# Kernel optimization log

Measured on AMD Instinct MI355X. Metric: run time of the kernel, lower is better.

The kernel has to match this reference:

```python
import jax, jax.numpy as jnp
import numpy as np

DEPTH = 12
N_FEATURES = 512
BATCH = 16384
N_NODES = 2 ** DEPTH - 1   # 4095 internal nodes, concatenated level-by-level
N_LEAVES = 2 ** DEPTH      # 4096


def setup_inputs() -> dict:
    key = jax.random.key(0)
    k_x, k_w, k_b, k_s, k_l = jax.random.split(key, 5)
    x_input = jax.random.normal(k_x, (BATCH, N_FEATURES), dtype=jnp.float32)
    # Per-level Linear(n_features, 2**d) weights concatenated on the output dim:
    # level d occupies rows [2**d - 1, 2**(d+1) - 1).
    bound = 1.0 / np.sqrt(N_FEATURES)  # torch Linear default init scale
    W_all = jax.random.uniform(k_w, (N_NODES, N_FEATURES), dtype=jnp.float32,
                               minval=-bound, maxval=bound)
    b_all = jax.random.uniform(k_b, (N_NODES,), dtype=jnp.float32,
                               minval=-bound, maxval=bound)
    # original uses max(randn, 1) -> positive steepness >= 1
    s_all = jax.random.uniform(k_s, (N_NODES,), dtype=jnp.float32,
                               minval=1.0, maxval=2.0)
    leaves = jax.random.normal(k_l, (N_LEAVES,), dtype=jnp.float32)
    return {"x_input": x_input, "W_all": W_all, "b_all": b_all,
            "s_all": s_all, "leaves": leaves}


def reference(x_input, W_all, b_all, s_all, leaves):
    B = x_input.shape[0]
    # One fused GEMM for all depth levels: [B, 2**depth - 1]
    logits = x_input @ W_all.T + b_all
    p_all = jax.nn.sigmoid(logits * s_all)
    # Recursive path-probability product down the binary tree.
    # out[:, j] at level d is the prob of reaching child j (j = 2*node + side),
    # matching the original dict insertion order (node ascending, left then right).
    out = jnp.ones((B, 1), dtype=p_all.dtype)
    for d in range(DEPTH):
        start = 2 ** d - 1
        p = p_all[:, start:start + 2 ** d]          # [B, 2**d]
        # interleave left (parent*p) and right (parent*(1-p)) children
        out = jnp.stack([out * p, out * (1.0 - p)], axis=-1).reshape(B, 2 ** (d + 1))
    # weighted sum over leaves
    return (jax.nn.sigmoid(leaves) * out).sum(axis=1)   # [B]
```

## Files before the change

kernel.cpp:

```cpp
#include <hip/hip_runtime.h>
#include <hip/hip_bf16.h>

#define M_DIM   16384
#define K_DIM   512
#define NNODES  4095
#define NPERM   4096
#define NTOP    128
#define NWROWS  (NPERM + NTOP)
#define NBOT_BLOCKS (32 * 128)
#define NTOT_BLOCKS (NBOT_BLOCKS + 128)

typedef __bf16   bf16x8 __attribute__((ext_vector_type(8)));
typedef float    floatx4 __attribute__((ext_vector_type(4)));

__device__ __forceinline__ float sigmoidf_(float z) {
    return __builtin_amdgcn_rcpf(1.f + __expf(-z));
}

__device__ __forceinline__ void gld_lds16(const void* g, void* l) {
    __builtin_amdgcn_global_load_lds(
        (const __attribute__((address_space(1))) void*)g,
        (__attribute__((address_space(3))) void*)l, 16, 0, 0);
}

__global__ __launch_bounds__(256) void cvt_all(const float* __restrict__ X,
                                               const float* __restrict__ W,
                                               const float* __restrict__ bias,
                                               const float* __restrict__ scale,
                                               __hip_bfloat16* __restrict__ Xb,
                                               __hip_bfloat16* __restrict__ Wb,
                                               float* __restrict__ bp,
                                               float* __restrict__ sp) {
    const int bid = blockIdx.x;
    if (bid < 4096) {
        const int idx = (bid * 256 + threadIdx.x) * 8;
        float4 f0 = *reinterpret_cast<const float4*>(X + idx);
        float4 f1 = *reinterpret_cast<const float4*>(X + idx + 4);
        __hip_bfloat16 h[8];
        h[0] = __float2bfloat16(f0.x); h[1] = __float2bfloat16(f0.y);
        h[2] = __float2bfloat16(f0.z); h[3] = __float2bfloat16(f0.w);
        h[4] = __float2bfloat16(f1.x); h[5] = __float2bfloat16(f1.y);
        h[6] = __float2bfloat16(f1.z); h[7] = __float2bfloat16(f1.w);
        *reinterpret_cast<int4*>(Xb + idx) = *reinterpret_cast<int4*>(h);
        return;
    }
    const int idx = ((bid - 4096) * 256 + threadIdx.x) * 8;
    const int r = idx >> 9;
    const int k = idx & 511;
    int node;
    if (r < NPERM) {
        const int t = r >> 5, o = r & 31;
        int d, q;
        if (o < 16)       { d = 11; q = o; }
        else if (o < 24)  { d = 10; q = o - 16; }
        else if (o < 28)  { d = 9;  q = o - 24; }
        else if (o < 30)  { d = 8;  q = o - 28; }
        else if (o == 30) { d = 7;  q = 0; }
        else              { d = -1; q = 0; }
        node = (d < 0) ? -1 : ((1 << d) - 1 + (t << (d - 7)) + q);
    } else {
        const int c = r - NPERM;
        node = (c < 127) ? c : -1;
    }
    __hip_bfloat16 h[8];
    if (node >= 0) {
        const float* src = W + (size_t)node * 512 + k;
        float4 f0 = *reinterpret_cast<const float4*>(src);
        float4 f1 = *reinterpret_cast<const float4*>(src + 4);
        h[0] = __float2bfloat16(f0.x); h[1] = __float2bfloat16(f0.y);
        h[2] = __float2bfloat16(f0.z); h[3] = __float2bfloat16(f0.w);
        h[4] = __float2bfloat16(f1.x); h[5] = __float2bfloat16(f1.y);
        h[6] = __float2bfloat16(f1.z); h[7] = __float2bfloat16(f1.w);
    } else {
        #pragma unroll
        for (int i = 0; i < 8; ++i) h[i] = __float2bfloat16(0.f);
    }
    *reinterpret_cast<int4*>(Wb + idx) = *reinterpret_cast<int4*>(h);
    if (k == 0) {
        bp[r] = (node >= 0) ? bias[node]  : 0.f;
        sp[r] = (node >= 0) ? scale[node] : 1.f;
    }
}

#define PT_STRIDE 135
#define BUFB 32768
__global__ __launch_bounds__(256) void gemm_fold(
    const __hip_bfloat16* __restrict__ A,
    const __hip_bfloat16* __restrict__ B,
    const float* __restrict__ bp,
    const float* __restrict__ sp,
    const float* __restrict__ leaves,
    float* __restrict__ partial,
    _Float16* __restrict__ ptop)
{
    __shared__ char smem[66560] __attribute__((aligned(16)));
    _Float16* pt  = (_Float16*)smem;
    float*    slf = (float*)(smem + 66048);

    const int tid  = threadIdx.x;
    const int lane = tid & 63;
    const int wv   = tid >> 6;
    const int bid  = blockIdx.x;
    int tile_m, tile_n;
    if (bid < NBOT_BLOCKS) { tile_m = bid >> 5; tile_n = bid & 31; }
    else                   { tile_m = bid - NBOT_BLOCKS; tile_n = 32; }
    const int m0 = tile_m * 128;
    const int n0 = tile_n * 128;

    if (tile_n < 32 && tid < 128) slf[tid] = sigmoidf_(leaves[n0 + tid]);

    const int wm = (wv >> 1) * 64;
    const int wn = (wv & 1) * 64;
    const int lrow = lane >> 3;
    const int swzb = ((lane & 7) ^ lrow) * 16;
    const int quad = lane >> 4;
    const int l15  = lane & 15;
    const int xr   = l15 & 7;

    const char* gAp[4];
    const char* gBp[4];
    char* sA[4];
    char* sB[4];
    #pragma unroll
    for (int i = 0; i < 4; ++i) {
        const int rbase = i * 32 + wv * 8;
        gAp[i] = (const char*)(A + (size_t)(m0 + rbase + lrow) * K_DIM) + swzb;
        gBp[i] = (const char*)(B + (size_t)(n0 + rbase + lrow) * K_DIM) + swzb;
        sA[i] = smem + rbase * 128;
        sB[i] = smem + 16384 + rbase * 128;
    }

    floatx4 acc[4][4];
    #pragma unroll
    for (int i = 0; i < 4; ++i)
        #pragma unroll
        for (int j = 0; j < 4; ++j)
            acc[i][j] = (floatx4){0.f, 0.f, 0.f, 0.f};

    #pragma unroll
    for (int i = 0; i < 4; ++i) {
        gld_lds16(gAp[i], sA[i]);
        gld_lds16(gBp[i], sB[i]);
        gAp[i] += 128; gBp[i] += 128;
    }

    #pragma unroll 1
    for (int k0 = 0; k0 < 8; ++k0) {
        __syncthreads();
        if (k0 < 7) {
            const int boff = ((k0 + 1) & 1) * BUFB;
            #pragma unroll
            for (int i = 0; i < 4; ++i) {
                gld_lds16(gAp[i], sA[i] + boff);
                gld_lds16(gBp[i], sB[i] + boff);
                gAp[i] += 128; gBp[i] += 128;
            }
        }
        const __hip_bfloat16* cA =
            (const __hip_bfloat16*)(smem + (k0 & 1) * BUFB);
        const __hip_bfloat16* cB = cA + 8192;
        #pragma unroll
        for (int kk = 0; kk < 64; kk += 32) {
            const int cb = ((kk >> 3) + quad) ^ xr;
            bf16x8 af[4], bfr[4];
            #pragma unroll
            for (int i = 0; i < 4; ++i)
                af[i] = *reinterpret_cast<const bf16x8*>(
                    &cA[(wm + i * 16 + l15) * 64 + cb * 8]);
            #pragma unroll
            for (int j = 0; j < 4; ++j)
                bfr[j] = *reinterpret_cast<const bf16x8*>(
                    &cB[(wn + j * 16 + l15) * 64 + cb * 8]);
            #pragma unroll
            for (int i = 0; i < 4; ++i)
                #pragma unroll
                for (int j = 0; j < 4; ++j)
                    acc[i][j] = __builtin_amdgcn_mfma_f32_16x16x32_bf16(
                        af[i], bfr[j], acc[i][j], 0, 0, 0);
        }
    }
    __syncthreads();

    float bn[4], sn[4];
    #pragma unroll
    for (int j = 0; j < 4; ++j) {
        const int n = n0 + wn + j * 16 + l15;
        bn[j] = bp[n];
        sn[j] = sp[n];
    }

    if (tile_n == 32) {
        #pragma unroll
        for (int i = 0; i < 4; ++i) {
            #pragma unroll
            for (int r = 0; r < 4; ++r) {
                const int m = m0 + wm + i * 16 + quad * 4 + r;
                #pragma unroll
                for (int j = 0; j < 4; ++j) {
                    const int col = wn + j * 16 + l15;
                    ptop[(size_t)m * 128 + col] =
                        (_Float16)sigmoidf_((acc[i][j][r] + bn[j]) * sn[j]);
                }
            }
        }
        return;
    }

    #pragma unroll
    for (int i = 0; i < 4; ++i) {
        #pragma unroll
        for (int r = 0; r < 4; ++r) {
            const int row = wm + i * 16 + quad * 4 + r;
            #pragma unroll
            for (int j = 0; j < 4; ++j) {
                const int col = wn + j * 16 + l15;
                pt[row * PT_STRIDE + col] =
                    (_Float16)sigmoidf_((acc[i][j][r] + bn[j]) * sn[j]);
            }
        }
    }
    __syncthreads();

    #pragma unroll
    for (int z = 0; z < 2; ++z) {
        const int task = tid + z * 256;
        const int row  = task >> 2;
        const int t    = task & 3;
        const _Float16* pp = pt + row * PT_STRIDE + t * 32;
        const float*    sl = slf + t * 32;
        float v[16];
        #pragma unroll
        for (int q = 0; q < 16; ++q) {
            const float p = (float)pp[q];
            v[q] = p * sl[2 * q] + (1.f - p) * sl[2 * q + 1];
        }
        #pragma unroll
        for (int q = 0; q < 8; ++q) {
            const float p = (float)pp[16 + q];
            v[q] = p * v[2 * q] + (1.f - p) * v[2 * q + 1];
        }
        #pragma unroll
        for (int q = 0; q < 4; ++q) {
            const float p = (float)pp[24 + q];
            v[q] = p * v[2 * q] + (1.f - p) * v[2 * q + 1];
        }
        #pragma unroll
        for (int q = 0; q < 2; ++q) {
            const float p = (float)pp[28 + q];
            v[q] = p * v[2 * q] + (1.f - p) * v[2 * q + 1];
        }
        const float p7 = (float)pp[30];
        partial[(size_t)(m0 + row) * 128 + tile_n * 4 + t] =
            p7 * v[0] + (1.f - p7) * v[1];
    }
}

__global__ __launch_bounds__(256) void final_fold(
    const float* __restrict__ partial,
    const _Float16* __restrict__ ptop,
    float* __restrict__ out)
{
    __shared__ float    pL[64 * 129];
    __shared__ _Float16 pq[64 * 134];

    const int tid = threadIdx.x;
    const int m0  = blockIdx.x * 64;

    #pragma unroll
    for (int it = 0; it < 32; ++it) {
        const int idx = tid + it * 256;
        const int row = idx >> 7;
        const int c   = idx & 127;
        pL[row * 129 + c] = partial[(size_t)(m0 + row) * 128 + c];
        pq[row * 134 + c] = ptop[(size_t)(m0 + row) * 128 + c];
    }
    __syncthreads();

    if (tid < 64) {
        float* v = pL + tid * 129;
        const _Float16* pr = pq + tid * 134;
        #pragma unroll
        for (int d = 6; d >= 1; --d) {
            const int base = (1 << d) - 1;
            const int cnt  = 1 << d;
            for (int q = 0; q < cnt; ++q) {
                const float p = (float)pr[base + q];
                v[q] = p * v[2 * q] + (1.f - p) * v[2 * q + 1];
            }
        }
        const float p0 = (float)pr[0];
        out[m0 + tid] = p0 * v[0] + (1.f - p0) * v[1];
    }
}

__global__ __launch_bounds__(256) void tnn_fallback(
    const float* __restrict__ X, const float* __restrict__ W,
    const float* __restrict__ bias, const float* __restrict__ scale,
    const float* __restrict__ leaves, float* __restrict__ out)
{
    __shared__ float xr[512];
    __shared__ float sl[4096];
    __shared__ float pp[4096];
    __shared__ float v0[2048];
    __shared__ float v1[1024];
    const int tid  = threadIdx.x;
    const int lane = tid & 63;
    const int wv   = tid >> 6;
    const int b    = blockIdx.x;
    for (int i = tid; i < 512;  i += 256) xr[i] = X[(size_t)b * 512 + i];
    for (int i = tid; i < 4096; i += 256) sl[i] = sigmoidf_(leaves[i]);
    __syncthreads();
    for (int n = wv; n < NNODES; n += 4) {
        float sum = 0.f;
        const float* wr = W + (size_t)n * 512;
        for (int k = lane; k < 512; k += 64) sum += xr[k] * wr[k];
        #pragma unroll
        for (int off = 32; off; off >>= 1) sum += __shfl_xor(sum, off);
        if (lane == 0) pp[n] = sigmoidf_((sum + bias[n]) * scale[n]);
    }
    __syncthreads();
    for (int j = tid; j < 2048; j += 256) {
        const float p = pp[2047 + j];
        v0[j] = p * sl[2 * j] + (1.f - p) * sl[2 * j + 1];
    }
    __syncthreads();
    float* src = v0;
    float* dst = v1;
    for (int d = 10; d >= 0; --d) {
        const int width = 1 << d;
        const int start = width - 1;
        for (int j = tid; j < width; j += 256) {
            const float p = pp[start + j];
            dst[j] = p * src[2 * j] + (1.f - p) * src[2 * j + 1];
        }
        __syncthreads();
        float* t = src; src = dst; dst = t;
    }
    if (tid == 0) out[b] = src[0];
}

extern "C" void kernel_launch(void* const* d_in, const int* in_sizes, int n_in,
                              void* d_out, int out_size, void* d_ws, size_t ws_size,
                              hipStream_t stream) {
    const float* X      = (const float*)d_in[0];
    const float* W      = (const float*)d_in[1];
    const float* bias   = (const float*)d_in[2];
    const float* scale  = (const float*)d_in[3];
    const float* leaves = (const float*)d_in[4];
    float* out = (float*)d_out;

    const size_t offX  = 0;
    const size_t offW  = (size_t)M_DIM * K_DIM * 2;
    const size_t offB  = offW + (size_t)NWROWS * K_DIM * 2;
    const size_t offS  = offB + (size_t)NWROWS * 4;
    const size_t offP  = offS + (size_t)NWROWS * 4;
    const size_t offT  = offP + (size_t)M_DIM * 128 * 4;
    const size_t need  = offT + (size_t)M_DIM * 128 * 2;

    if (ws_size >= need) {
        __hip_bfloat16* Xb = (__hip_bfloat16*)((char*)d_ws + offX);
        __hip_bfloat16* Wb = (__hip_bfloat16*)((char*)d_ws + offW);
        float* bp = (float*)((char*)d_ws + offB);
        float* sp = (float*)((char*)d_ws + offS);
        float* partial = (float*)((char*)d_ws + offP);
        _Float16* ptop = (_Float16*)((char*)d_ws + offT);
        cvt_all<<<4096 + 1056, 256, 0, stream>>>(X, W, bias, scale, Xb, Wb, bp, sp);
        gemm_fold<<<NTOT_BLOCKS, 256, 0, stream>>>(
            Xb, Wb, bp, sp, leaves, partial, ptop);
        final_fold<<<M_DIM / 64, 256, 0, stream>>>(partial, ptop, out);
    } else {
        tnn_fallback<<<M_DIM, 256, 0, stream>>>(X, W, bias, scale, leaves, out);
    }
}
```

Measured before the change: 190.4 us.

## Use 256x128 tiles with 512 threads and a triple-buffered LDS ring

Each GEMM block now covers a 256x128 output tile with 8 waves instead of 128x128 with 4 waves. The two-buffer K loop becomes a three-stage LDS ring, with partial vmcnt waits, the next-stage loads split across two half-steps, and s_setprio raised around the MFMA bursts. The goal is better reuse of B tiles and more overlap of global loads with MFMA work. In exchange it raises LDS use to about 147KB, limiting each CU to one block, and adds more barriers per K step.

```diff
diff --git a/kernel.cpp b/kernel.cpp
--- a/kernel.cpp
+++ b/kernel.cpp
@@ -7,8 +7,13 @@
 #define NPERM   4096
 #define NTOP    128
 #define NWROWS  (NPERM + NTOP)
-#define NBOT_BLOCKS (32 * 128)
-#define NTOT_BLOCKS (NBOT_BLOCKS + 128)
+
+#define NBOT_BLOCKS (64 * 32)
+#define NTOT_BLOCKS (NBOT_BLOCKS + 64)
+#define RING    49152
+#define SLF_OFF (3 * RING)
+#define SMEM_BYTES (SLF_OFF + 512)
+#define PT_STRIDE 135
 
 typedef __bf16   bf16x8 __attribute__((ext_vector_type(8)));
 typedef float    floatx4 __attribute__((ext_vector_type(4)));
@@ -82,9 +87,7 @@
     }
 }
 
-#define PT_STRIDE 135
-#define BUFB 32768
-__global__ __launch_bounds__(256) void gemm_fold(
+__global__ __launch_bounds__(512, 1) void gemm_fold(
     const __hip_bfloat16* __restrict__ A,
     const __hip_bfloat16* __restrict__ B,
     const float* __restrict__ bp,
@@ -93,9 +96,9 @@
     float* __restrict__ partial,
     _Float16* __restrict__ ptop)
 {
-    __shared__ char smem[66560] __attribute__((aligned(16)));
+    __shared__ char smem[SMEM_BYTES] __attribute__((aligned(16)));
     _Float16* pt  = (_Float16*)smem;
-    float*    slf = (float*)(smem + 66048);
+    float*    slf = (float*)(smem + SLF_OFF);
 
     const int tid  = threadIdx.x;
     const int lane = tid & 63;
@@ -104,10 +107,8 @@
     int tile_m, tile_n;
     if (bid < NBOT_BLOCKS) { tile_m = bid >> 5; tile_n = bid & 31; }
     else                   { tile_m = bid - NBOT_BLOCKS; tile_n = 32; }
-    const int m0 = tile_m * 128;
+    const int m0 = tile_m * 256;
     const int n0 = tile_n * 128;
-
-    if (tile_n < 32 && tid < 128) slf[tid] = sigmoidf_(leaves[n0 + tid]);
 
     const int wm = (wv >> 1) * 64;
     const int wn = (wv & 1) * 64;
@@ -118,16 +119,20 @@
     const int xr   = l15 & 7;
 
     const char* gAp[4];
-    const char* gBp[4];
+    const char* gBp[2];
     char* sA[4];
-    char* sB[4];
+    char* sB[2];
     #pragma unroll
     for (int i = 0; i < 4; ++i) {
-        const int rbase = i * 32 + wv * 8;
+        const int rbase = i * 64 + wv * 8;
         gAp[i] = (const char*)(A + (size_t)(m0 + rbase + lrow) * K_DIM) + swzb;
-        gBp[i] = (const char*)(B + (size_t)(n0 + rbase + lrow) * K_DIM) + swzb;
-        sA[i] = smem + rbase * 128;
-        sB[i] = smem + 16384 + rbase * 128;
+        sA[i]  = smem + rbase * 128;
+    }
+    #pragma unroll
+    for (int j = 0; j < 2; ++j) {
+        const int rbase = j * 64 + wv * 8;
+        gBp[j] = (const char*)(B + (size_t)(n0 + rbase + lrow) * K_DIM) + swzb;
+        sB[j]  = smem + 32768 + rbase * 128;
     }
 
     floatx4 acc[4][4];
@@ -138,30 +143,25 @@
             acc[i][j] = (floatx4){0.f, 0.f, 0.f, 0.f};
 
     #pragma unroll
-    for (int i = 0; i < 4; ++i) {
-        gld_lds16(gAp[i], sA[i]);
-        gld_lds16(gBp[i], sB[i]);
-        gAp[i] += 128; gBp[i] += 128;
-    }
-
+    for (int i = 0; i < 4; ++i) { gld_lds16(gAp[i], sA[i]); gAp[i] += 128; }
+    #pragma unroll
+    for (int j = 0; j < 2; ++j) { gld_lds16(gBp[j], sB[j]); gBp[j] += 128; }
+    #pragma unroll
+    for (int i = 0; i < 4; ++i) { gld_lds16(gAp[i], sA[i] + RING); gAp[i] += 128; }
+    #pragma unroll
+    for (int j = 0; j < 2; ++j) { gld_lds16(gBp[j], sB[j] + RING); gBp[j] += 128; }
+    asm volatile("s_waitcnt vmcnt(6)" ::: "memory");
+    __builtin_amdgcn_s_barrier();
+
+    int cur = 0;
+    int stg = 2 * RING;
     #pragma unroll 1
-    for (int k0 = 0; k0 < 8; ++k0) {
-        __syncthreads();
-        if (k0 < 7) {
-            const int boff = ((k0 + 1) & 1) * BUFB;
-            #pragma unroll
-            for (int i = 0; i < 4; ++i) {
-                gld_lds16(gAp[i], sA[i] + boff);
-                gld_lds16(gBp[i], sB[i] + boff);
-                gAp[i] += 128; gBp[i] += 128;
-            }
-        }
-        const __hip_bfloat16* cA =
-            (const __hip_bfloat16*)(smem + (k0 & 1) * BUFB);
-        const __hip_bfloat16* cB = cA + 8192;
-        #pragma unroll
-        for (int kk = 0; kk < 64; kk += 32) {
-            const int cb = ((kk >> 3) + quad) ^ xr;
+    for (int t = 0; t < 8; ++t) {
+        const __hip_bfloat16* cA = (const __hip_bfloat16*)(smem + cur);
+        const __hip_bfloat16* cB = (const __hip_bfloat16*)(smem + cur + 32768);
+
+        {
+            const int cb = quad ^ xr;
             bf16x8 af[4], bfr[4];
             #pragma unroll
             for (int i = 0; i < 4; ++i)
@@ -171,13 +171,61 @@
             for (int j = 0; j < 4; ++j)
                 bfr[j] = *reinterpret_cast<const bf16x8*>(
                     &cB[(wn + j * 16 + l15) * 64 + cb * 8]);
+            if (t < 6) {
+                gld_lds16(gAp[0], sA[0] + stg);
+                gld_lds16(gAp[1], sA[1] + stg);
+                gld_lds16(gBp[0], sB[0] + stg);
+            }
+            __builtin_amdgcn_s_barrier();
+            __builtin_amdgcn_s_setprio(1);
             #pragma unroll
             for (int i = 0; i < 4; ++i)
                 #pragma unroll
                 for (int j = 0; j < 4; ++j)
                     acc[i][j] = __builtin_amdgcn_mfma_f32_16x16x32_bf16(
                         af[i], bfr[j], acc[i][j], 0, 0, 0);
-        }
+            __builtin_amdgcn_s_setprio(0);
+            __builtin_amdgcn_s_barrier();
+        }
+
+        {
+            const int cb = (4 + quad) ^ xr;
+            bf16x8 af[4], bfr[4];
+            #pragma unroll
+            for (int i = 0; i < 4; ++i)
+                af[i] = *reinterpret_cast<const bf16x8*>(
+                    &cA[(wm + i * 16 + l15) * 64 + cb * 8]);
+            #pragma unroll
+            for (int j = 0; j < 4; ++j)
+                bfr[j] = *reinterpret_cast<const bf16x8*>(
+                    &cB[(wn + j * 16 + l15) * 64 + cb * 8]);
+            if (t < 6) {
+                gld_lds16(gAp[2], sA[2] + stg);
+                gld_lds16(gAp[3], sA[3] + stg);
+                gld_lds16(gBp[1], sB[1] + stg);
+                #pragma unroll
+                for (int i = 0; i < 4; ++i) gAp[i] += 128;
+                gBp[0] += 128; gBp[1] += 128;
+            }
+            __builtin_amdgcn_s_barrier();
+            __builtin_amdgcn_s_setprio(1);
+            #pragma unroll
+            for (int i = 0; i < 4; ++i)
+                #pragma unroll
+                for (int j = 0; j < 4; ++j)
+                    acc[i][j] = __builtin_amdgcn_mfma_f32_16x16x32_bf16(
+                        af[i], bfr[j], acc[i][j], 0, 0, 0);
+            __builtin_amdgcn_s_setprio(0);
+            if (t < 6) {
+                asm volatile("s_waitcnt vmcnt(6)" ::: "memory");
+            } else if (t == 6) {
+                asm volatile("s_waitcnt vmcnt(0)" ::: "memory");
+            }
+            __builtin_amdgcn_s_barrier();
+        }
+
+        cur = (cur == 2 * RING) ? 0 : cur + RING;
+        stg = (stg == 2 * RING) ? 0 : stg + RING;
     }
     __syncthreads();
 
@@ -206,6 +254,8 @@
         return;
     }
 
+    if (tid < 128) slf[tid] = sigmoidf_(leaves[n0 + tid]);
+
     #pragma unroll
     for (int i = 0; i < 4; ++i) {
         #pragma unroll
@@ -223,11 +273,11 @@
 
     #pragma unroll
     for (int z = 0; z < 2; ++z) {
-        const int task = tid + z * 256;
+        const int task = tid + z * 512;
         const int row  = task >> 2;
-        const int t    = task & 3;
-        const _Float16* pp = pt + row * PT_STRIDE + t * 32;
-        const float*    sl = slf + t * 32;
+        const int st   = task & 3;
+        const _Float16* pp = pt + row * PT_STRIDE + st * 32;
+        const float*    sl = slf + st * 32;
         float v[16];
         #pragma unroll
         for (int q = 0; q < 16; ++q) {
@@ -250,7 +300,7 @@
             v[q] = p * v[2 * q] + (1.f - p) * v[2 * q + 1];
         }
         const float p7 = (float)pp[30];
-        partial[(size_t)(m0 + row) * 128 + tile_n * 4 + t] =
+        partial[(size_t)(m0 + row) * 128 + tile_n * 4 + st] =
             p7 * v[0] + (1.f - p7) * v[1];
     }
 }
@@ -365,7 +415,7 @@
         float* partial = (float*)((char*)d_ws + offP);
         _Float16* ptop = (_Float16*)((char*)d_ws + offT);
         cvt_all<<<4096 + 1056, 256, 0, stream>>>(X, W, bias, scale, Xb, Wb, bp, sp);
-        gemm_fold<<<NTOT_BLOCKS, 256, 0, stream>>>(
+        gemm_fold<<<NTOT_BLOCKS, 512, 0, stream>>>(
             Xb, Wb, bp, sp, leaves, partial, ptop);
         final_fold<<<M_DIM / 64, 256, 0, stream>>>(partial, ptop, out);
     } else {
```

New measurement: 224.3 us. +17.8%, slower.

## Enlarge GEMM tile to 256x128 with K-step 32 and two blocks per CU

Applied to the files above, without the earlier changes.

The fused GEMM+fold kernel now computes 256x128 output tiles, with each wave owning 128x64, and walks K in 32-wide steps over 16 iterations. LDS per block shrinks to about 69 KB with a new 4-way swizzle, and launch_bounds requests 2 blocks per CU. The aim is to raise arithmetic intensity per A/B load and improve occupancy and latency hiding. In exchange, each thread keeps twice as many accumulators (128 floats), which adds register pressure, and there are twice as many barriers per block.

```diff
diff --git a/kernel.cpp b/kernel.cpp
--- a/kernel.cpp
+++ b/kernel.cpp
@@ -7,8 +7,13 @@
 #define NPERM   4096
 #define NTOP    128
 #define NWROWS  (NPERM + NTOP)
-#define NBOT_BLOCKS (32 * 128)
-#define NTOT_BLOCKS (NBOT_BLOCKS + 128)
+
+#define NBOT_BLOCKS (64 * 32)
+#define NTOT_BLOCKS (NBOT_BLOCKS + 64)
+#define BUFB    24576
+#define PT_STRIDE 135
+#define SLF_OFF (256 * PT_STRIDE * 2)
+#define SMEM_BYTES (SLF_OFF + 512)
 
 typedef __bf16   bf16x8 __attribute__((ext_vector_type(8)));
 typedef float    floatx4 __attribute__((ext_vector_type(4)));
@@ -82,9 +87,7 @@
     }
 }
 
-#define PT_STRIDE 135
-#define BUFB 32768
-__global__ __launch_bounds__(256) void gemm_fold(
+__global__ __launch_bounds__(256, 2) void gemm_fold(
     const __hip_bfloat16* __restrict__ A,
     const __hip_bfloat16* __restrict__ B,
     const float* __restrict__ bp,
@@ -93,9 +96,9 @@
     float* __restrict__ partial,
     _Float16* __restrict__ ptop)
 {
-    __shared__ char smem[66560] __attribute__((aligned(16)));
+    __shared__ char smem[SMEM_BYTES] __attribute__((aligned(16)));
     _Float16* pt  = (_Float16*)smem;
-    float*    slf = (float*)(smem + 66048);
+    float*    slf = (float*)(smem + SLF_OFF);
 
     const int tid  = threadIdx.x;
     const int lane = tid & 63;
@@ -104,79 +107,75 @@
     int tile_m, tile_n;
     if (bid < NBOT_BLOCKS) { tile_m = bid >> 5; tile_n = bid & 31; }
     else                   { tile_m = bid - NBOT_BLOCKS; tile_n = 32; }
-    const int m0 = tile_m * 128;
+    const int m0 = tile_m * 256;
     const int n0 = tile_n * 128;
 
     if (tile_n < 32 && tid < 128) slf[tid] = sigmoidf_(leaves[n0 + tid]);
 
-    const int wm = (wv >> 1) * 64;
-    const int wn = (wv & 1) * 64;
-    const int lrow = lane >> 3;
-    const int swzb = ((lane & 7) ^ lrow) * 16;
+    const int wvm = wv >> 1;
+    const int wvn = wv & 1;
     const int quad = lane >> 4;
     const int l15  = lane & 15;
-    const int xr   = l15 & 7;
-
+    const int cbS  = (quad ^ (l15 & 3)) * 8;
+
+    const int srow = lane >> 2;
+    const int swz  = (((lane & 3) ^ (srow & 3)) * 16);
     const char* gAp[4];
-    const char* gBp[4];
+    const char* gBp[2];
     char* sA[4];
-    char* sB[4];
-    #pragma unroll
-    for (int i = 0; i < 4; ++i) {
-        const int rbase = i * 32 + wv * 8;
-        gAp[i] = (const char*)(A + (size_t)(m0 + rbase + lrow) * K_DIM) + swzb;
-        gBp[i] = (const char*)(B + (size_t)(n0 + rbase + lrow) * K_DIM) + swzb;
-        sA[i] = smem + rbase * 128;
-        sB[i] = smem + 16384 + rbase * 128;
-    }
-
-    floatx4 acc[4][4];
-    #pragma unroll
-    for (int i = 0; i < 4; ++i)
+    char* sB[2];
+    #pragma unroll
+    for (int c = 0; c < 4; ++c) {
+        const int rbase = c * 64 + wv * 16;
+        gAp[c] = (const char*)(A + (size_t)(m0 + rbase + srow) * K_DIM) + swz;
+        sA[c]  = smem + rbase * 64;
+    }
+    #pragma unroll
+    for (int c = 0; c < 2; ++c) {
+        const int rbase = c * 64 + wv * 16;
+        gBp[c] = (const char*)(B + (size_t)(n0 + rbase + srow) * K_DIM) + swz;
+        sB[c]  = smem + 16384 + rbase * 64;
+    }
+
+    floatx4 acc[8][4];
+    #pragma unroll
+    for (int i = 0; i < 8; ++i)
         #pragma unroll
         for (int j = 0; j < 4; ++j)
             acc[i][j] = (floatx4){0.f, 0.f, 0.f, 0.f};
 
     #pragma unroll
-    for (int i = 0; i < 4; ++i) {
-        gld_lds16(gAp[i], sA[i]);
-        gld_lds16(gBp[i], sB[i]);
-        gAp[i] += 128; gBp[i] += 128;
-    }
+    for (int c = 0; c < 4; ++c) { gld_lds16(gAp[c], sA[c]); gAp[c] += 64; }
+    #pragma unroll
+    for (int c = 0; c < 2; ++c) { gld_lds16(gBp[c], sB[c]); gBp[c] += 64; }
 
     #pragma unroll 1
-    for (int k0 = 0; k0 < 8; ++k0) {
+    for (int k0 = 0; k0 < 16; ++k0) {
         __syncthreads();
-        if (k0 < 7) {
+        if (k0 < 15) {
             const int boff = ((k0 + 1) & 1) * BUFB;
             #pragma unroll
-            for (int i = 0; i < 4; ++i) {
-                gld_lds16(gAp[i], sA[i] + boff);
-                gld_lds16(gBp[i], sB[i] + boff);
-                gAp[i] += 128; gBp[i] += 128;
-            }
+            for (int c = 0; c < 4; ++c) { gld_lds16(gAp[c], sA[c] + boff); gAp[c] += 64; }
+            #pragma unroll
+            for (int c = 0; c < 2; ++c) { gld_lds16(gBp[c], sB[c] + boff); gBp[c] += 64; }
         }
         const __hip_bfloat16* cA =
             (const __hip_bfloat16*)(smem + (k0 & 1) * BUFB);
         const __hip_bfloat16* cB = cA + 8192;
-        #pragma unroll
-        for (int kk = 0; kk < 64; kk += 32) {
-            const int cb = ((kk >> 3) + quad) ^ xr;
-            bf16x8 af[4], bfr[4];
-            #pragma unroll
-            for (int i = 0; i < 4; ++i)
-                af[i] = *reinterpret_cast<const bf16x8*>(
-                    &cA[(wm + i * 16 + l15) * 64 + cb * 8]);
+
+        bf16x8 bfr[4];
+        #pragma unroll
+        for (int j = 0; j < 4; ++j)
+            bfr[j] = *reinterpret_cast<const bf16x8*>(
+                &cB[(wvn * 64 + j * 16 + l15) * 32 + cbS]);
+        #pragma unroll
+        for (int i = 0; i < 8; ++i) {
+            const bf16x8 af = *reinterpret_cast<const bf16x8*>(
+                &cA[(wvm * 128 + i * 16 + l15) * 32 + cbS]);
             #pragma unroll
             for (int j = 0; j < 4; ++j)
-                bfr[j] = *reinterpret_cast<const bf16x8*>(
-                    &cB[(wn + j * 16 + l15) * 64 + cb * 8]);
-            #pragma unroll
-            for (int i = 0; i < 4; ++i)
-                #pragma unroll
-                for (int j = 0; j < 4; ++j)
-                    acc[i][j] = __builtin_amdgcn_mfma_f32_16x16x32_bf16(
-                        af[i], bfr[j], acc[i][j], 0, 0, 0);
+                acc[i][j] = __builtin_amdgcn_mfma_f32_16x16x32_bf16(
+                    af, bfr[j], acc[i][j], 0, 0, 0);
         }
     }
     __syncthreads();
@@ -184,20 +183,20 @@
     float bn[4], sn[4];
     #pragma unroll
     for (int j = 0; j < 4; ++j) {
-        const int n = n0 + wn + j * 16 + l15;
+        const int n = n0 + wvn * 64 + j * 16 + l15;
         bn[j] = bp[n];
         sn[j] = sp[n];
     }
 
     if (tile_n == 32) {
         #pragma unroll
-        for (int i = 0; i < 4; ++i) {
+        for (int i = 0; i < 8; ++i) {
             #pragma unroll
             for (int r = 0; r < 4; ++r) {
-                const int m = m0 + wm + i * 16 + quad * 4 + r;
+                const int m = m0 + wvm * 128 + i * 16 + quad * 4 + r;
                 #pragma unroll
                 for (int j = 0; j < 4; ++j) {
-                    const int col = wn + j * 16 + l15;
+                    const int col = wvn * 64 + j * 16 + l15;
                     ptop[(size_t)m * 128 + col] =
                         (_Float16)sigmoidf_((acc[i][j][r] + bn[j]) * sn[j]);
                 }
@@ -207,13 +206,13 @@
     }
 
     #pragma unroll
-    for (int i = 0; i < 4; ++i) {
+    for (int i = 0; i < 8; ++i) {
         #pragma unroll
         for (int r = 0; r < 4; ++r) {
-            const int row = wm + i * 16 + quad * 4 + r;
+            const int row = wvm * 128 + i * 16 + quad * 4 + r;
             #pragma unroll
             for (int j = 0; j < 4; ++j) {
-                const int col = wn + j * 16 + l15;
+                const int col = wvn * 64 + j * 16 + l15;
                 pt[row * PT_STRIDE + col] =
                     (_Float16)sigmoidf_((acc[i][j][r] + bn[j]) * sn[j]);
             }
@@ -222,12 +221,12 @@
     __syncthreads();
 
     #pragma unroll
-    for (int z = 0; z < 2; ++z) {
+    for (int z = 0; z < 4; ++z) {
         const int task = tid + z * 256;
         const int row  = task >> 2;
-        const int t    = task & 3;
-        const _Float16* pp = pt + row * PT_STRIDE + t * 32;
-        const float*    sl = slf + t * 32;
+        const int st   = task & 3;
+        const _Float16* pp = pt + row * PT_STRIDE + st * 32;
+        const float*    sl = slf + st * 32;
         float v[16];
         #pragma unroll
         for (int q = 0; q < 16; ++q) {
@@ -250,7 +249,7 @@
             v[q] = p * v[2 * q] + (1.f - p) * v[2 * q + 1];
         }
         const float p7 = (float)pp[30];
-        partial[(size_t)(m0 + row) * 128 + tile_n * 4 + t] =
+        partial[(size_t)(m0 + row) * 128 + tile_n * 4 + st] =
             p7 * v[0] + (1.f - p7) * v[1];
     }
 }
```

Result: slower. 195.0 us (+2.4%).

## Fuse final fold into GEMM kernel via last-block atomic counter per row tile

Applied to the files above, without the earlier changes.

Removes the separate final_fold launch. Each gemm_fold block bumps an atomic counter for its row tile, and the 33rd block to finish a tile runs the top-level fold for its 128 rows in two passes. Counters are zeroed in cvt_all. This saves one kernel launch and the gap between kernels, at the cost of threadfences, an atomic per block, and a serialized tail fold done by one block per row tile.

```diff
diff --git a/kernel.cpp b/kernel.cpp
--- a/kernel.cpp
+++ b/kernel.cpp
@@ -30,9 +30,11 @@
                                                __hip_bfloat16* __restrict__ Xb,
                                                __hip_bfloat16* __restrict__ Wb,
                                                float* __restrict__ bp,
-                                               float* __restrict__ sp) {
+                                               float* __restrict__ sp,
+                                               int* __restrict__ cnt) {
     const int bid = blockIdx.x;
     if (bid < 4096) {
+        if (bid == 0 && threadIdx.x < 128) cnt[threadIdx.x] = 0;
         const int idx = (bid * 256 + threadIdx.x) * 8;
         float4 f0 = *reinterpret_cast<const float4*>(X + idx);
         float4 f1 = *reinterpret_cast<const float4*>(X + idx + 4);
@@ -91,9 +93,12 @@
     const float* __restrict__ sp,
     const float* __restrict__ leaves,
     float* __restrict__ partial,
-    _Float16* __restrict__ ptop)
+    _Float16* __restrict__ ptop,
+    float* __restrict__ out,
+    int* __restrict__ cnt)
 {
     __shared__ char smem[66560] __attribute__((aligned(16)));
+    __shared__ int lastflag;
     _Float16* pt  = (_Float16*)smem;
     float*    slf = (float*)(smem + 66048);
 
@@ -203,93 +208,96 @@
                 }
             }
         }
-        return;
-    }
-
-    #pragma unroll
-    for (int i = 0; i < 4; ++i) {
-        #pragma unroll
-        for (int r = 0; r < 4; ++r) {
-            const int row = wm + i * 16 + quad * 4 + r;
-            #pragma unroll
-            for (int j = 0; j < 4; ++j) {
-                const int col = wn + j * 16 + l15;
-                pt[row * PT_STRIDE + col] =
-                    (_Float16)sigmoidf_((acc[i][j][r] + bn[j]) * sn[j]);
-            }
-        }
-    }
-    __syncthreads();
-
-    #pragma unroll
-    for (int z = 0; z < 2; ++z) {
-        const int task = tid + z * 256;
-        const int row  = task >> 2;
-        const int t    = task & 3;
-        const _Float16* pp = pt + row * PT_STRIDE + t * 32;
-        const float*    sl = slf + t * 32;
-        float v[16];
-        #pragma unroll
-        for (int q = 0; q < 16; ++q) {
-            const float p = (float)pp[q];
-            v[q] = p * sl[2 * q] + (1.f - p) * sl[2 * q + 1];
-        }
-        #pragma unroll
-        for (int q = 0; q < 8; ++q) {
-            const float p = (float)pp[16 + q];
-            v[q] = p * v[2 * q] + (1.f - p) * v[2 * q + 1];
-        }
-        #pragma unroll
-        for (int q = 0; q < 4; ++q) {
-            const float p = (float)pp[24 + q];
-            v[q] = p * v[2 * q] + (1.f - p) * v[2 * q + 1];
-        }
-        #pragma unroll
-        for (int q = 0; q < 2; ++q) {
-            const float p = (float)pp[28 + q];
-            v[q] = p * v[2 * q] + (1.f - p) * v[2 * q + 1];
-        }
-        const float p7 = (float)pp[30];
-        partial[(size_t)(m0 + row) * 128 + tile_n * 4 + t] =
-            p7 * v[0] + (1.f - p7) * v[1];
-    }
-}
-
-__global__ __launch_bounds__(256) void final_fold(
-    const float* __restrict__ partial,
-    const _Float16* __restrict__ ptop,
-    float* __restrict__ out)
-{
-    __shared__ float    pL[64 * 129];
-    __shared__ _Float16 pq[64 * 134];
-
-    const int tid = threadIdx.x;
-    const int m0  = blockIdx.x * 64;
-
-    #pragma unroll
-    for (int it = 0; it < 32; ++it) {
-        const int idx = tid + it * 256;
-        const int row = idx >> 7;
-        const int c   = idx & 127;
-        pL[row * 129 + c] = partial[(size_t)(m0 + row) * 128 + c];
-        pq[row * 134 + c] = ptop[(size_t)(m0 + row) * 128 + c];
-    }
-    __syncthreads();
-
-    if (tid < 64) {
-        float* v = pL + tid * 129;
-        const _Float16* pr = pq + tid * 134;
-        #pragma unroll
-        for (int d = 6; d >= 1; --d) {
-            const int base = (1 << d) - 1;
-            const int cnt  = 1 << d;
-            for (int q = 0; q < cnt; ++q) {
-                const float p = (float)pr[base + q];
+    } else {
+        #pragma unroll
+        for (int i = 0; i < 4; ++i) {
+            #pragma unroll
+            for (int r = 0; r < 4; ++r) {
+                const int row = wm + i * 16 + quad * 4 + r;
+                #pragma unroll
+                for (int j = 0; j < 4; ++j) {
+                    const int col = wn + j * 16 + l15;
+                    pt[row * PT_STRIDE + col] =
+                        (_Float16)sigmoidf_((acc[i][j][r] + bn[j]) * sn[j]);
+                }
+            }
+        }
+        __syncthreads();
+
+        #pragma unroll
+        for (int z = 0; z < 2; ++z) {
+            const int task = tid + z * 256;
+            const int row  = task >> 2;
+            const int t    = task & 3;
+            const _Float16* pp = pt + row * PT_STRIDE + t * 32;
+            const float*    sl = slf + t * 32;
+            float v[16];
+            #pragma unroll
+            for (int q = 0; q < 16; ++q) {
+                const float p = (float)pp[q];
+                v[q] = p * sl[2 * q] + (1.f - p) * sl[2 * q + 1];
+            }
+            #pragma unroll
+            for (int q = 0; q < 8; ++q) {
+                const float p = (float)pp[16 + q];
                 v[q] = p * v[2 * q] + (1.f - p) * v[2 * q + 1];
             }
-        }
-        const float p0 = (float)pr[0];
-        out[m0 + tid] = p0 * v[0] + (1.f - p0) * v[1];
+            #pragma unroll
+            for (int q = 0; q < 4; ++q) {
+                const float p = (float)pp[24 + q];
+                v[q] = p * v[2 * q] + (1.f - p) * v[2 * q + 1];
+            }
+            #pragma unroll
+            for (int q = 0; q < 2; ++q) {
+                const float p = (float)pp[28 + q];
+                v[q] = p * v[2 * q] + (1.f - p) * v[2 * q + 1];
+            }
+            const float p7 = (float)pp[30];
+            partial[(size_t)(m0 + row) * 128 + tile_n * 4 + t] =
+                p7 * v[0] + (1.f - p7) * v[1];
+        }
+    }
+
+    __threadfence();
+    __syncthreads();
+    if (tid == 0) {
+        const int prev = atomicAdd(cnt + tile_m, 1);
+        lastflag = (prev == 32) ? 1 : 0;
+    }
+    __syncthreads();
+    if (lastflag == 0) return;
+    __threadfence();
+
+    float*    fL = (float*)smem;
+    _Float16* fq = (_Float16*)(smem + 64 * 129 * 4);
+    #pragma unroll 1
+    for (int pass = 0; pass < 2; ++pass) {
+        const int r0 = m0 + pass * 64;
+        __syncthreads();
+        #pragma unroll
+        for (int it = 0; it < 32; ++it) {
+            const int idx = tid + it * 256;
+            const int row = idx >> 7;
+            const int c   = idx & 127;
+            fL[row * 129 + c] = partial[(size_t)(r0 + row) * 128 + c];
+            fq[row * 134 + c] = ptop[(size_t)(r0 + row) * 128 + c];
+        }
+        __syncthreads();
+        if (tid < 64) {
+            float* v = fL + tid * 129;
+            const _Float16* pr = fq + tid * 134;
+            #pragma unroll
+            for (int d = 6; d >= 1; --d) {
+                const int base = (1 << d) - 1;
+                const int cw   = 1 << d;
+                for (int q = 0; q < cw; ++q) {
+                    const float p = (float)pr[base + q];
+                    v[q] = p * v[2 * q] + (1.f - p) * v[2 * q + 1];
+                }
+            }
+            const float p0 = (float)pr[0];
+            out[r0 + tid] = p0 * v[0] + (1.f - p0) * v[1];
+        }
     }
 }
 
@@ -355,7 +363,8 @@
     const size_t offS  = offB + (size_t)NWROWS * 4;
     const size_t offP  = offS + (size_t)NWROWS * 4;
     const size_t offT  = offP + (size_t)M_DIM * 128 * 4;
-    const size_t need  = offT + (size_t)M_DIM * 128 * 2;
+    const size_t offC  = offT + (size_t)M_DIM * 128 * 2;
+    const size_t need  = offC + 512;
 
     if (ws_size >= need) {
         __hip_bfloat16* Xb = (__hip_bfloat16*)((char*)d_ws + offX);
@@ -364,10 +373,10 @@
         float* sp = (float*)((char*)d_ws + offS);
         float* partial = (float*)((char*)d_ws + offP);
         _Float16* ptop = (_Float16*)((char*)d_ws + offT);
-        cvt_all<<<4096 + 1056, 256, 0, stream>>>(X, W, bias, scale, Xb, Wb, bp, sp);
+        int* cnt = (int*)((char*)d_ws + offC);
+        cvt_all<<<4096 + 1056, 256, 0, stream>>>(X, W, bias, scale, Xb, Wb, bp, sp, cnt);
         gemm_fold<<<NTOT_BLOCKS, 256, 0, stream>>>(
-            Xb, Wb, bp, sp, leaves, partial, ptop);
-        final_fold<<<M_DIM / 64, 256, 0, stream>>>(partial, ptop, out);
+            Xb, Wb, bp, sp, leaves, partial, ptop, out, cnt);
     } else {
         tnn_fallback<<<M_DIM, 256, 0, stream>>>(X, W, bias, scale, leaves, out);
     }
```

Result: slower. 633.3 us (+232.5%).
